# Performance work log

Measured on AMD Instinct MI355X. Metric: run time of the kernel, lower is better.

## Reference

```python
import jax, jax.numpy as jnp
import numpy as np

EMBED_DIM = 1024
NUM_HEADS = 16
EFF_HEADS = NUM_HEADS // 2
HEAD_DIM = EMBED_DIM // NUM_HEADS
LAMBDA_INIT = 0.8
B, N = 2, 2048


def setup_inputs() -> dict:
    key = jax.random.key(0)
    ks = jax.random.split(key, 14)
    s = 0.02
    return {
        "x": jax.random.normal(ks[0], (B, N, EMBED_DIM), dtype=jnp.float32),
        "Wq": jax.random.normal(ks[1], (EMBED_DIM, EMBED_DIM), dtype=jnp.float32) * s,
        "bq": jnp.zeros((EMBED_DIM,), dtype=jnp.float32),
        "Wk": jax.random.normal(ks[2], (EMBED_DIM, EMBED_DIM), dtype=jnp.float32) * s,
        "bk": jnp.zeros((EMBED_DIM,), dtype=jnp.float32),
        "Wv": jax.random.normal(ks[3], (EMBED_DIM, EMBED_DIM), dtype=jnp.float32) * s,
        "bv": jnp.zeros((EMBED_DIM,), dtype=jnp.float32),
        "Wp": jax.random.normal(ks[4], (EMBED_DIM, EMBED_DIM), dtype=jnp.float32) * s,
        "bp": jnp.zeros((EMBED_DIM,), dtype=jnp.float32),
        "lambda_q1": jax.random.normal(ks[5], (EFF_HEADS, 1, HEAD_DIM), dtype=jnp.float32) * s,
        "lambda_k1": jax.random.normal(ks[6], (EFF_HEADS, 1, HEAD_DIM), dtype=jnp.float32) * s,
        "lambda_q2": jax.random.normal(ks[7], (EFF_HEADS, 1, HEAD_DIM), dtype=jnp.float32) * s,
        "lambda_k2": jax.random.normal(ks[8], (EFF_HEADS, 1, HEAD_DIM), dtype=jnp.float32) * s,
    }


def reference(x, Wq, bq, Wk, bk, Wv, bv, Wp, bp,
              lambda_q1, lambda_k1, lambda_q2, lambda_k2):
    Bb, Nn, C = x.shape
    H, H2, hd = NUM_HEADS, EFF_HEADS, HEAD_DIM
    scale = hd ** (-0.5)

    # projections (torch Linear: y = x @ W.T + b), reshape to [B,H,N,hd]
    q = (x @ Wq.T + bq).reshape(Bb, Nn, H, hd).transpose(0, 2, 1, 3)
    k = (x @ Wk.T + bk).reshape(Bb, Nn, H, hd).transpose(0, 2, 1, 3)
    v = (x @ Wv.T + bv).reshape(Bb, Nn, H, hd).transpose(0, 2, 1, 3)

    q1, q2 = q[:, :H2], q[:, H2:]
    k1, k2 = k[:, :H2], k[:, H2:]
    v1, v2 = v[:, :H2], v[:, H2:]

    # scalar lambda: per-head dot products, clamped exp, differenced, averaged
    l1 = jnp.exp(jnp.minimum((lambda_q1 * lambda_k1).sum((-1, -2)), 5.0))  # [H2]
    l2 = jnp.exp(jnp.minimum((lambda_q2 * lambda_k2).sum((-1, -2)), 5.0))
    lv = (l1 - l2 + LAMBDA_INIT).mean()

    a1 = jax.nn.softmax(jnp.einsum('bhnd,bhmd->bhnm', q1, k1) * scale, axis=-1)
    x1 = jnp.einsum('bhnm,bhmd->bhnd', a1, v1).transpose(0, 2, 1, 3).reshape(Bb, Nn, C // 2)
    a2 = jax.nn.softmax(jnp.einsum('bhnd,bhmd->bhnm', q2, k2) * scale, axis=-1)
    x2 = jnp.einsum('bhnm,bhmd->bhnd', a2, v2).transpose(0, 2, 1, 3).reshape(Bb, Nn, C // 2)

    out = jnp.concatenate([x1 - lv * x2, x2], axis=-1) @ Wp.T + bp
    return out
```

## Files before the change

### kernel.cpp

```cpp
#include <hip/hip_runtime.h>

typedef __bf16 bf16;
typedef __bf16 bf16x8 __attribute__((ext_vector_type(8)));
typedef __bf16 bf16x4 __attribute__((ext_vector_type(4)));
typedef float  f32x16 __attribute__((ext_vector_type(16)));
typedef unsigned int uint;
typedef unsigned int uintx4 __attribute__((ext_vector_type(4)));

#define QSCALE (0.125f * 1.44269504088896340736f)

__device__ __forceinline__ void g2l16(const void* g, void* l) {
  __builtin_amdgcn_global_load_lds(
      (const __attribute__((address_space(1))) void*)g,
      (__attribute__((address_space(3))) void*)l, 16, 0, 0);
}

__device__ __forceinline__ f32x16 mfma16(bf16x8 a, bf16x8 b, f32x16 c) {
  return __builtin_amdgcn_mfma_f32_32x32x16_bf16(a, b, c, 0, 0, 0);
}

__device__ __forceinline__ uint pack_bf16(float a, float b) {
  unsigned short lo = __builtin_bit_cast(unsigned short, (bf16)a);
  unsigned short hi = __builtin_bit_cast(unsigned short, (bf16)b);
  return (uint)lo | ((uint)hi << 16);
}

__global__ void cast5_kernel(const float* __restrict__ x,
                             const float* __restrict__ wq, const float* __restrict__ wk,
                             const float* __restrict__ wv, const float* __restrict__ wp,
                             const float* __restrict__ lq1, const float* __restrict__ lk1,
                             const float* __restrict__ lq2, const float* __restrict__ lk2,
                             bf16* __restrict__ xb, bf16* __restrict__ wqkv,
                             bf16* __restrict__ wpb) {
  int seg = blockIdx.y;
  long i = (long)(blockIdx.x * 256 + threadIdx.x) * 8;
  const float* s; bf16* d; long n;
  if (seg == 0)      { s = x;  d = xb;  n = 4194304; }
  else if (seg == 1) { s = wq; d = wqkv;            n = 1048576; }
  else if (seg == 2) { s = wk; d = wqkv + 1048576;  n = 1048576; }
  else if (seg == 3) { s = wv; d = wqkv + 2097152;  n = 1048576; }
  else               { s = wp; d = wpb;             n = 1048576; }
  if (i >= n) return;
  float4 f0 = *(const float4*)(s + i);
  float4 f1 = *(const float4*)(s + i + 4);
  if (seg == 4 && (i & 1023) >= 512) {
    int t = threadIdx.x & 63;
    float accum = 0.f;
    for (int hh = 0; hh < 8; ++hh) {
      float v1 = lq1[hh*64 + t] * lk1[hh*64 + t];
      float v2 = lq2[hh*64 + t] * lk2[hh*64 + t];
      for (int off = 32; off; off >>= 1) {
        v1 += __shfl_xor(v1, off);
        v2 += __shfl_xor(v2, off);
      }
      accum += expf(fminf(v1, 5.f)) - expf(fminf(v2, 5.f));
    }
    float lv = accum / 8.f + 0.8f;
    float4 g0 = *(const float4*)(s + i - 512);
    float4 g1 = *(const float4*)(s + i - 508);
    f0.x -= lv * g0.x; f0.y -= lv * g0.y; f0.z -= lv * g0.z; f0.w -= lv * g0.w;
    f1.x -= lv * g1.x; f1.y -= lv * g1.y; f1.z -= lv * g1.z; f1.w -= lv * g1.w;
  }
  bf16x8 o;
  o[0] = (bf16)f0.x; o[1] = (bf16)f0.y; o[2] = (bf16)f0.z; o[3] = (bf16)f0.w;
  o[4] = (bf16)f1.x; o[5] = (bf16)f1.y; o[6] = (bf16)f1.z; o[7] = (bf16)f1.w;
  *(bf16x8*)(d + i) = o;
}

__global__ __launch_bounds__(256, 2) void gemm_qkv_kernel(
    const bf16* __restrict__ A, const bf16* __restrict__ B,
    const float* __restrict__ bias0, const float* __restrict__ bias1,
    const float* __restrict__ bias2,
    bf16* __restrict__ O0, bf16* __restrict__ O1, bf16* __restrict__ O2) {
  __shared__ __align__(16) char smem[32 * 1024];
  const int tid = threadIdx.x;
  const int w = tid >> 6, L = tid & 63;
  const int l31 = L & 31, h5 = L >> 5;
  const int m0 = blockIdx.x * 128;
  const int n0g = blockIdx.y * 128;
  const int by = n0g >> 10;
  const bf16* Bp = B + (long)by * 1048576;
  const float* biasp = (by == 0) ? bias0 : ((by == 1) ? bias1 : bias2);
  const int nloc = n0g & 1023;

  f32x16 acc[2][2];
  for (int i = 0; i < 2; ++i) for (int j = 0; j < 2; ++j)
    for (int r = 0; r < 16; ++r) acc[i][j][r] = 0.f;

  const int srow = L >> 1, spar = L & 1;
  const int wm = w >> 1, wn = w & 1;
  const int fs = (l31 * 2 + h5) * 16;

  for (int k0 = 0; k0 < 1024; k0 += 64) {
    for (int i = 0; i < 8; ++i) {
      int r = w * 8 + i;
      int rr = r & 15;
      int rowblk = rr >> 2, kst = rr & 3;
      int row = rowblk * 32 + srow;
      int kk = k0 + (kst * 2 + spar) * 8;
      const bf16* gsrc = (r < 16) ? (A + (long)(m0 + row) * 1024 + kk)
                                  : (Bp + (long)(nloc + row) * 1024 + kk);
      g2l16(gsrc, smem + r * 1024);
    }
    __syncthreads();
    for (int kst = 0; kst < 4; ++kst) {
      bf16x8 a0 = *(const bf16x8*)(smem + (((wm * 2 + 0) * 4 + kst) * 1024) + fs);
      bf16x8 a1 = *(const bf16x8*)(smem + (((wm * 2 + 1) * 4 + kst) * 1024) + fs);
      bf16x8 b0 = *(const bf16x8*)(smem + 16384 + (((wn * 2 + 0) * 4 + kst) * 1024) + fs);
      bf16x8 b1 = *(const bf16x8*)(smem + 16384 + (((wn * 2 + 1) * 4 + kst) * 1024) + fs);
      acc[0][0] = mfma16(a0, b0, acc[0][0]);
      acc[0][1] = mfma16(a0, b1, acc[0][1]);
      acc[1][0] = mfma16(a1, b0, acc[1][0]);
      acc[1][1] = mfma16(a1, b1, acc[1][1]);
    }
    __syncthreads();
  }

  if (by == 2) {
    int b = m0 >> 11;
    int nbase = (m0 & 2047);
    for (int mi = 0; mi < 2; ++mi) for (int ni = 0; ni < 2; ++ni) {
      int col = nloc + wn * 64 + ni * 32 + l31;
      int hh = col >> 6, d = col & 63;
      float bias_v = biasp[col];
      long rowbase = ((long)(b * 16 + hh) * 64 + d) * 2048 + nbase + wm * 64;
      for (int g = 0; g < 4; ++g) {
        bf16x4 pk;
        for (int r = 0; r < 4; ++r) pk[r] = (bf16)(acc[mi][ni][g * 4 + r] + bias_v);
        int Qp = mi * 4 + g;
        int slot = (Qp >> 1) * 16 + h5 * 8 + (Qp & 1) * 4;
        *(bf16x4*)(O2 + rowbase + slot) = pk;
      }
    }
  } else {
    bf16* dst = (by == 0) ? O0 : O1;
    float scale = (by == 0) ? QSCALE : 1.0f;
    for (int mi = 0; mi < 2; ++mi) for (int ni = 0; ni < 2; ++ni) {
      int col = nloc + wn * 64 + ni * 32 + l31;
      float bias_v = biasp[col];
      int row_base = m0 + wm * 64 + mi * 32 + 4 * h5;
      for (int reg = 0; reg < 16; ++reg) {
        int rowoff = (reg & 3) + 8 * (reg >> 2);
        float v = (acc[mi][ni][reg] + bias_v) * scale;
        dst[(long)(row_base + rowoff) * 1024 + col] = (bf16)v;
      }
    }
  }
}

__global__ __launch_bounds__(256, 2) void gemm_proj_kernel(
    const bf16* __restrict__ A, const bf16* __restrict__ B,
    const float* __restrict__ bias, float* __restrict__ Of) {
  __shared__ __align__(16) char smem[24 * 1024];
  const int tid = threadIdx.x;
  const int w = tid >> 6, L = tid & 63;
  const int l31 = L & 31, h5 = L >> 5;
  const int m0 = blockIdx.x * 64;
  const int nloc = blockIdx.y * 128;

  f32x16 acc[2];
  for (int i = 0; i < 2; ++i)
    for (int r = 0; r < 16; ++r) acc[i][r] = 0.f;

  const int srow = L >> 1, spar = L & 1;
  const int fs = (l31 * 2 + h5) * 16;

  for (int k0 = 0; k0 < 1024; k0 += 64) {
    for (int i = 0; i < 6; ++i) {
      int r = w * 6 + i;
      const bf16* gsrc;
      if (r < 8) {
        int rowblk = r >> 2, kst = r & 3;
        gsrc = A + (long)(m0 + rowblk * 32 + srow) * 1024 + k0 + (kst * 2 + spar) * 8;
      } else {
        int rr = r - 8;
        int rowblk = rr >> 2, kst = rr & 3;
        gsrc = B + (long)(nloc + rowblk * 32 + srow) * 1024 + k0 + (kst * 2 + spar) * 8;
      }
      g2l16(gsrc, smem + r * 1024);
    }
    __syncthreads();
    for (int kst = 0; kst < 4; ++kst) {
      bf16x8 a0 = *(const bf16x8*)(smem + ((0 * 4 + kst) * 1024) + fs);
      bf16x8 a1 = *(const bf16x8*)(smem + ((1 * 4 + kst) * 1024) + fs);
      bf16x8 bb = *(const bf16x8*)(smem + 8192 + ((w * 4 + kst) * 1024) + fs);
      acc[0] = mfma16(a0, bb, acc[0]);
      acc[1] = mfma16(a1, bb, acc[1]);
    }
    __syncthreads();
  }

  for (int mi = 0; mi < 2; ++mi) {
    int col = nloc + w * 32 + l31;
    float bias_v = bias[col];
    int row_base = m0 + mi * 32 + 4 * h5;
    for (int reg = 0; reg < 16; ++reg) {
      int rowoff = (reg & 3) + 8 * (reg >> 2);
      Of[(long)(row_base + rowoff) * 1024 + col] = acc[mi][reg] + bias_v;
    }
  }
}

__global__ __launch_bounds__(512, 4) void attn_kernel(
    const bf16* __restrict__ Qb, const bf16* __restrict__ Kb,
    const bf16* __restrict__ Vt, bf16* __restrict__ Ob) {
  __shared__ __align__(16) char smem[34816];
  const int tid = threadIdx.x, w = tid >> 6, L = tid & 63;
  const int half = w >> 2, pair = w & 3;
  const int bh = blockIdx.x, qt = blockIdx.y;
  const int b = bh >> 4, h = bh & 15;
  const int q0 = qt * 128 + pair * 32;
  const int l31 = L & 31, h5 = L >> 5;
  const int srow = L >> 1, spar = L & 1;
  const int fs = (l31 * 2 + h5) * 16;
  char* kbase = smem + half * 16384;

  bf16x8 qf[4];
  for (int kst = 0; kst < 4; ++kst)
    qf[kst] = *(const bf16x8*)(Qb + (long)(b * 2048 + q0 + l31) * 1024 + h * 64
                               + kst * 16 + h5 * 8);

  f32x16 o[2];
  for (int i = 0; i < 2; ++i)
    for (int r = 0; r < 16; ++r) o[i][r] = 0.f;
  float ls[4] = {0.f, 0.f, 0.f, 0.f};

  const bf16* Kbh = Kb + (long)b * 2048 * 1024 + h * 64 + (long)half * 1024 * 1024;
  const bf16* Vth = Vt + (long)bh * 64 * 2048 + half * 1024;

  for (int t = 0; t < 16; ++t) {
    int n0 = t * 64;
    for (int i = 0; i < 4; ++i) {
      int r = pair * 4 + i;
      if (r < 8) {
        int nkb = r >> 2, kst = r & 3;
        const bf16* g = Kbh + (long)(n0 + nkb * 32 + srow) * 1024 + (kst * 2 + spar) * 8;
        g2l16(g, kbase + r * 1024);
      } else {
        int rr = r - 8, db = rr >> 2, kst = rr & 3;
        const bf16* g = Vth + (long)(db * 32 + srow) * 2048 + n0 + (kst * 2 + spar) * 8;
        g2l16(g, kbase + 8192 + rr * 1024);
      }
    }
    __syncthreads();

    f32x16 s[2];
    for (int i = 0; i < 2; ++i)
      for (int r = 0; r < 16; ++r) s[i][r] = 0.f;
    for (int kst = 0; kst < 4; ++kst) {
      bf16x8 k0f = *(const bf16x8*)(kbase + (kst * 1024) + fs);
      bf16x8 k1f = *(const bf16x8*)(kbase + ((4 + kst) * 1024) + fs);
      s[0] = mfma16(k0f, qf[kst], s[0]);
      s[1] = mfma16(k1f, qf[kst], s[1]);
    }

    for (int nki = 0; nki < 2; ++nki)
      for (int r = 0; r < 16; ++r) {
        float p = __builtin_amdgcn_exp2f(s[nki][r]);
        s[nki][r] = p;
        ls[r & 3] += p;
      }

    for (int kst = 0; kst < 4; ++kst) {
      bf16x8 v0 = *(const bf16x8*)(kbase + 8192 + (kst * 1024) + fs);
      bf16x8 v1 = *(const bf16x8*)(kbase + 8192 + ((4 + kst) * 1024) + fs);
      int nki = kst >> 1;
      int rbase = (kst & 1) * 8;
      uintx4 uv;
      uv.x = pack_bf16(s[nki][rbase + 0], s[nki][rbase + 1]);
      uv.y = pack_bf16(s[nki][rbase + 2], s[nki][rbase + 3]);
      uv.z = pack_bf16(s[nki][rbase + 4], s[nki][rbase + 5]);
      uv.w = pack_bf16(s[nki][rbase + 6], s[nki][rbase + 7]);
      bf16x8 pf = __builtin_bit_cast(bf16x8, uv);
      o[0] = mfma16(v0, pf, o[0]);
      o[1] = mfma16(v1, pf, o[1]);
    }
    __syncthreads();
  }

  float lsum = (ls[0] + ls[1]) + (ls[2] + ls[3]);
  float lcol = lsum + __shfl_xor(lsum, 32);
  if (half) {
    float* dstO = (float*)smem + pair * 2112;
    for (int di = 0; di < 2; ++di)
      for (int r = 0; r < 16; ++r) dstO[L * 33 + di * 16 + r] = o[di][r];
    if (h5 == 0) ((float*)(smem + 33792))[pair * 32 + l31] = lcol;
  }
  __syncthreads();
  float linv = 0.f;
  if (!half) {
    float* srcO = (float*)smem + pair * 2112;
    for (int di = 0; di < 2; ++di)
      for (int r = 0; r < 16; ++r) o[di][r] += srcO[L * 33 + di * 16 + r];
    float lother = ((float*)(smem + 33792))[pair * 32 + l31];
    linv = 1.f / (lcol + lother);
  }
  __syncthreads();
  if (!half) {
    char* ot = smem + pair * 4352;
    for (int di = 0; di < 2; ++di)
      for (int g = 0; g < 4; ++g) {
        bf16x4 pk;
        for (int r = 0; r < 4; ++r)
          pk[r] = (bf16)(o[di][g * 4 + r] * linv);
        int d0 = di * 32 + g * 8 + h5 * 4;
        *(bf16x4*)(ot + (l31 * 68 + d0) * 2) = pk;
      }
    for (int i = 0; i < 4; ++i) {
      int qloc = (L >> 3) + i * 8;
      int cc = L & 7;
      bf16x8 vv = *(const bf16x8*)(ot + (qloc * 68 + cc * 8) * 2);
      *(bf16x8*)(Ob + (long)(b * 2048 + q0 + qloc) * 1024 + h * 64 + cc * 8) = vv;
    }
  }
}

extern "C" void kernel_launch(void* const* d_in, const int* in_sizes, int n_in,
                              void* d_out, int out_size, void* d_ws, size_t ws_size,
                              hipStream_t stream) {
  const float* x   = (const float*)d_in[0];
  const float* Wq  = (const float*)d_in[1];
  const float* bq  = (const float*)d_in[2];
  const float* Wk  = (const float*)d_in[3];
  const float* bk  = (const float*)d_in[4];
  const float* Wv  = (const float*)d_in[5];
  const float* bv  = (const float*)d_in[6];
  const float* Wp  = (const float*)d_in[7];
  const float* bp  = (const float*)d_in[8];
  const float* lq1 = (const float*)d_in[9];
  const float* lk1 = (const float*)d_in[10];
  const float* lq2 = (const float*)d_in[11];
  const float* lk2 = (const float*)d_in[12];
  float* out = (float*)d_out;

  char* ws = (char*)d_ws;
  bf16* xb   = (bf16*)(ws + 1024);
  bf16* Wqkv = xb + (long)4096 * 1024;
  bf16* Wpb  = Wqkv + (long)3 * 1024 * 1024;
  bf16* Vt   = Wpb + (long)1024 * 1024;
  bf16* Ob   = Vt + (long)4096 * 1024;
  bf16* Qb = (bf16*)d_out;
  bf16* Kb = Qb + (long)4096 * 1024;

  cast5_kernel<<<dim3(2048, 5), 256, 0, stream>>>(
      x, Wq, Wk, Wv, Wp, lq1, lk1, lq2, lk2, xb, Wqkv, Wpb);
  gemm_qkv_kernel<<<dim3(32, 24), 256, 0, stream>>>(
      xb, Wqkv, bq, bk, bv, Qb, Kb, Vt);
  attn_kernel<<<dim3(32, 16), 512, 0, stream>>>(Qb, Kb, Vt, Ob);
  gemm_proj_kernel<<<dim3(64, 8), 256, 0, stream>>>(Ob, Wpb, bp, out);
}
```

Before: 208.8 us.

## Double-buffer K/V tiles in attention with async global-to-LDS prefetch

```diff
diff --git a/kernel.cpp b/kernel.cpp
--- a/kernel.cpp
+++ b/kernel.cpp
@@ -204,7 +204,7 @@
 __global__ __launch_bounds__(512, 4) void attn_kernel(
     const bf16* __restrict__ Qb, const bf16* __restrict__ Kb,
     const bf16* __restrict__ Vt, bf16* __restrict__ Ob) {
-  __shared__ __align__(16) char smem[34816];
+  __shared__ __align__(16) char smem[65536];
   const int tid = threadIdx.x, w = tid >> 6, L = tid & 63;
   const int half = w >> 2, pair = w & 3;
   const int bh = blockIdx.x, qt = blockIdx.y;
@@ -213,7 +213,6 @@
   const int l31 = L & 31, h5 = L >> 5;
   const int srow = L >> 1, spar = L & 1;
   const int fs = (l31 * 2 + h5) * 16;
-  char* kbase = smem + half * 16384;
 
   bf16x8 qf[4];
   for (int kst = 0; kst < 4; ++kst)
@@ -228,28 +227,45 @@
   const bf16* Kbh = Kb + (long)b * 2048 * 1024 + h * 64 + (long)half * 1024 * 1024;
   const bf16* Vth = Vt + (long)bh * 64 * 2048 + half * 1024;
 
-  for (int t = 0; t < 16; ++t) {
+  char* kb0 = smem + half * 16384;
+  char* kb1 = smem + 32768 + half * 16384;
+
+  auto stage = [&](int t, char* kb) {
     int n0 = t * 64;
     for (int i = 0; i < 4; ++i) {
       int r = pair * 4 + i;
       if (r < 8) {
         int nkb = r >> 2, kst = r & 3;
         const bf16* g = Kbh + (long)(n0 + nkb * 32 + srow) * 1024 + (kst * 2 + spar) * 8;
-        g2l16(g, kbase + r * 1024);
+        g2l16(g, kb + r * 1024);
       } else {
         int rr = r - 8, db = rr >> 2, kst = rr & 3;
         const bf16* g = Vth + (long)(db * 32 + srow) * 2048 + n0 + (kst * 2 + spar) * 8;
-        g2l16(g, kbase + 8192 + rr * 1024);
-      }
-    }
-    __syncthreads();
+        g2l16(g, kb + 8192 + rr * 1024);
+      }
+    }
+  };
+
+  stage(0, kb0);
+  stage(1, kb1);
+
+  for (int t = 0; t < 16; ++t) {
+    char* kb = (t & 1) ? kb1 : kb0;
+    if (t < 15) asm volatile("s_waitcnt vmcnt(4)" ::: "memory");
+    else        asm volatile("s_waitcnt vmcnt(0)" ::: "memory");
+    __builtin_amdgcn_s_barrier();
 
     f32x16 s[2];
-    for (int i = 0; i < 2; ++i)
-      for (int r = 0; r < 16; ++r) s[i][r] = 0.f;
-    for (int kst = 0; kst < 4; ++kst) {
-      bf16x8 k0f = *(const bf16x8*)(kbase + (kst * 1024) + fs);
-      bf16x8 k1f = *(const bf16x8*)(kbase + ((4 + kst) * 1024) + fs);
+    {
+      bf16x8 k0f = *(const bf16x8*)(kb + fs);
+      bf16x8 k1f = *(const bf16x8*)(kb + 4 * 1024 + fs);
+      f32x16 z = {};
+      s[0] = mfma16(k0f, qf[0], z);
+      s[1] = mfma16(k1f, qf[0], z);
+    }
+    for (int kst = 1; kst < 4; ++kst) {
+      bf16x8 k0f = *(const bf16x8*)(kb + (kst * 1024) + fs);
+      bf16x8 k1f = *(const bf16x8*)(kb + ((4 + kst) * 1024) + fs);
       s[0] = mfma16(k0f, qf[kst], s[0]);
       s[1] = mfma16(k1f, qf[kst], s[1]);
     }
@@ -262,8 +278,8 @@
       }
 
     for (int kst = 0; kst < 4; ++kst) {
-      bf16x8 v0 = *(const bf16x8*)(kbase + 8192 + (kst * 1024) + fs);
-      bf16x8 v1 = *(const bf16x8*)(kbase + 8192 + ((4 + kst) * 1024) + fs);
+      bf16x8 v0 = *(const bf16x8*)(kb + 8192 + (kst * 1024) + fs);
+      bf16x8 v1 = *(const bf16x8*)(kb + 8192 + ((4 + kst) * 1024) + fs);
       int nki = kst >> 1;
       int rbase = (kst & 1) * 8;
       uintx4 uv;
@@ -275,7 +291,9 @@
       o[0] = mfma16(v0, pf, o[0]);
       o[1] = mfma16(v1, pf, o[1]);
     }
-    __syncthreads();
+
+    __builtin_amdgcn_s_barrier();
+    if (t + 2 < 16) stage(t + 2, kb);
   }
 
   float lsum = (ls[0] + ls[1]) + (ls[2] + ls[3]);
```

Result: faster. 203.7 us (-2.5%).
